# Kernel tuning notes

Hardware: AMD Instinct MI355X
Metric: run time of the kernel (lower is better)

## Reference

```python
import jax, jax.numpy as jnp
import numpy as np

B, N, HID, E, H = 4, 256, 256, 64, 4
OUT = HID // 2          # 128
D = OUT // H            # 32
AGG = H * (2 * D + 1)   # 260 = concat(mean D, attn_sum 1, max D) per head


def setup_inputs() -> dict:
    key = jax.random.key(0)
    ks = jax.random.split(key, 7)
    s = 0.05
    return {
        "h_x": jax.random.normal(ks[0], (B, N, HID), jnp.float32),
        "h_e": jax.random.normal(ks[1], (B, N, N, E), jnp.float32),
        "h_m": jnp.ones((B, N), jnp.float32),
        "W_Q": jax.random.normal(ks[2], (OUT, HID), jnp.float32) * s,
        "W_K": jax.random.normal(ks[3], (OUT, E), jnp.float32) * s,
        "W_V": jax.random.normal(ks[4], (OUT, E), jnp.float32) * s,
        "W_R": jax.random.normal(ks[5], (OUT, AGG), jnp.float32) * s,
    }


def reference(h_x, h_e, h_m, W_Q, W_K, W_V, W_R):
    # queries from node features: [B,H,N,D]
    h_q = (h_x @ W_Q.T).reshape(B, N, H, D).transpose(0, 2, 1, 3)
    # keys/values from dense pairwise edge features: [B,H,N,N,D]
    h_k = jnp.einsum('bnme,ce->bnmc', h_e, W_K).reshape(B, N, N, H, D).transpose(0, 3, 1, 2, 4)
    h_v = jnp.einsum('bnme,ce->bnmc', h_e, W_V).reshape(B, N, N, H, D).transpose(0, 3, 1, 2, 4)
    # broadcast dot: [B,H,N,N]
    scores = jnp.einsum('bhnd,bhnmd->bhnm', h_q, h_k) / np.float32(np.sqrt(D))
    # per-node mask broadcast as [B,1,N,1] (masks query rows)
    scores = jnp.where(h_m[:, None, :, None] == 0, -jnp.inf, scores)
    # NOTE: original code softmaxes over dim=1 = HEAD axis (faithful)
    attn = jax.nn.softmax(scores, axis=1)                      # [B,H,N,N]
    attn_w = attn[..., None] * h_v                             # [B,H,N,N,D]
    aggr_sum = attn_w.sum(axis=3)                              # [B,H,N,D]
    attn_sum = attn.sum(axis=3, keepdims=True) + 1e-8          # [B,H,N,1]
    aggr_mean = aggr_sum / attn_sum
    aggr_max = attn_w.max(axis=3)                              # [B,H,N,D]
    multi = jnp.concatenate([aggr_mean, attn_sum, aggr_max], axis=-1)  # [B,H,N,2D+1]
    aggr_out = multi.transpose(0, 2, 1, 3).reshape(B, N, AGG)  # [B,N,260]
    return aggr_out @ W_R.T                                    # [B,N,OUT]
```

## Files before the change

### kernel.cpp

```cpp
#include <hip/hip_runtime.h>
#include <hip/hip_bf16.h>

constexpr int Bb   = 4;
constexpr int Nn   = 256;
constexpr int HID  = 256;
constexpr int Ee   = 64;
constexpr int Hh   = 4;
constexpr int OUTc = 128;
constexpr int Dd   = 32;
constexpr int AGG  = 260;
constexpr int REC  = 264;
constexpr int QA_LD = 264;

constexpr size_t WS_WRT   = 0;
constexpr size_t WS_FRAGV = WS_WRT + (size_t)AGG * OUTc;
constexpr size_t WS_FRAGQ = WS_FRAGV + 4096;
constexpr size_t WS_UFRAG = WS_FRAGQ + 16384;

typedef __attribute__((ext_vector_type(8))) short short8;
typedef __attribute__((ext_vector_type(4))) float floatx4;

__device__ __forceinline__ unsigned pk2(float a, float b) {
    union { __hip_bfloat162 h; unsigned u; } cv;
    cv.h = __float22bfloat162_rn(float2{a, b});
    return cv.u;
}

__device__ __forceinline__ short8 pack8(floatx4 f0, floatx4 f1) {
    union { short8 s; unsigned u[4]; } r;
    r.u[0] = pk2(f0[0], f0[1]);
    r.u[1] = pk2(f0[2], f0[3]);
    r.u[2] = pk2(f1[0], f1[1]);
    r.u[3] = pk2(f1[2], f1[3]);
    return r.s;
}

__device__ __forceinline__ void gload16(const float* g, float* l) {
    __builtin_amdgcn_global_load_lds(
        (const __attribute__((address_space(1))) void*)g,
        (__attribute__((address_space(3))) void*)l, 16, 0, 0);
}

__global__ __launch_bounds__(256)
void eama_prep(const float* __restrict__ W_Q, const float* __restrict__ W_V,
               const float* __restrict__ W_R, const float* __restrict__ h_x,
               const float* __restrict__ W_K,
               unsigned short* __restrict__ wfragV, float* __restrict__ W_RT,
               unsigned short* __restrict__ ufrag)
{
    __shared__ __align__(16) unsigned short sA[16 * QA_LD];
    __shared__ __align__(16) float sqL[16][132];
    __shared__ __align__(16) float sU2[16][256];

    const int tid = threadIdx.x;
    const int bid = blockIdx.x;

    if (bid < 4) {
        const int e    = bid * 256 + tid;
        const int lane = e & 63;
        const int ks   = (e >> 6) & 1;
        const int ct   = e >> 7;
        const int ncol = lane & 15, q8 = lane >> 4;
        const float* row = W_V + (ct * 16 + ncol) * Ee;
        const int k0 = ks * 32 + q8 * 8;
        floatx4 f0 = *(const floatx4*)(row + k0);
        floatx4 f1 = *(const floatx4*)(row + k0 + 4);
        *(short8*)(wfragV + (size_t)e * 8) = pack8(f0, f1);
        return;
    }
    if (bid < 134) {
        const int i = (bid - 4) * 256 + tid;
        if (i < AGG * OUTc) {
            const int c = i & 127, j = i >> 7;
            W_RT[j * OUTc + c] = W_R[c * AGG + j];
        }
        return;
    }

    const int b0   = (bid - 134) * 16;
    const int lane = tid & 63;
    const int wv   = tid >> 6;
    const int ncol = lane & 15, q8 = lane >> 4;

    short8 bq[2][8];
    #pragma unroll
    for (int ct = 0; ct < 2; ++ct)
        #pragma unroll
        for (int ks = 0; ks < 8; ++ks) {
            const float* row = W_Q + (size_t)(wv * 32 + ct * 16 + ncol) * HID + ks * 32 + q8 * 8;
            bq[ct][ks] = pack8(*(const floatx4*)row, *(const floatx4*)(row + 4));
        }
    #pragma unroll
    for (int i = 0; i < 2; ++i) {
        const int idx = tid + i * 256;
        const int r = idx >> 5, blk = idx & 31;
        const float* src = h_x + (size_t)(b0 + r) * HID + blk * 8;
        floatx4 f0 = *(const floatx4*)(src);
        floatx4 f1 = *(const floatx4*)(src + 4);
        *(short8*)&sA[r * QA_LD + blk * 8] = pack8(f0, f1);
    }
    __syncthreads();
    floatx4 acc[2] = {(floatx4){0,0,0,0}, (floatx4){0,0,0,0}};
    #pragma unroll
    for (int ks = 0; ks < 8; ++ks) {
        short8 a = *(const short8*)&sA[ncol * QA_LD + ks * 32 + q8 * 8];
        acc[0] = __builtin_amdgcn_mfma_f32_16x16x32_bf16(a, bq[0][ks], acc[0], 0, 0, 0);
        acc[1] = __builtin_amdgcn_mfma_f32_16x16x32_bf16(a, bq[1][ks], acc[1], 0, 0, 0);
    }
    #pragma unroll
    for (int ct = 0; ct < 2; ++ct)
        #pragma unroll
        for (int rr = 0; rr < 4; ++rr)
            sqL[q8 * 4 + rr][wv * 32 + ct * 16 + ncol] = acc[ct][rr];
    __syncthreads();

    {
        const int h = wv, e = lane;
        float a16[16];
        #pragma unroll
        for (int i = 0; i < 16; ++i) a16[i] = 0.f;
        #pragma unroll
        for (int d4 = 0; d4 < 8; ++d4) {
            float wk0 = W_K[(h * Dd + d4 * 4 + 0) * Ee + e];
            float wk1 = W_K[(h * Dd + d4 * 4 + 1) * Ee + e];
            float wk2 = W_K[(h * Dd + d4 * 4 + 2) * Ee + e];
            float wk3 = W_K[(h * Dd + d4 * 4 + 3) * Ee + e];
            #pragma unroll
            for (int b16 = 0; b16 < 16; ++b16) {
                floatx4 qv = *(const floatx4*)&sqL[b16][h * Dd + d4 * 4];
                a16[b16] += (qv[0] * wk0 + qv[1] * wk1) + (qv[2] * wk2 + qv[3] * wk3);
            }
        }
        #pragma unroll
        for (int b16 = 0; b16 < 16; ++b16)
            sU2[b16][h * 64 + e] = a16[b16] * (0.1767766952966369f * 1.4426950408889634f);
    }
    __syncthreads();

    #pragma unroll
    for (int k = 0; k < 8; ++k) {
        const int ei   = tid + k * 256;
        const int b16  = ei >> 7;
        const int rest = ei & 127;
        const int ks   = rest >> 6;
        const int l    = rest & 63;
        const int nc   = l & 15, qq = l >> 4;
        short8 v = {0, 0, 0, 0, 0, 0, 0, 0};
        if (nc < Hh) {
            floatx4 f0 = *(const floatx4*)&sU2[b16][nc * 64 + ks * 32 + qq * 8];
            floatx4 f1 = *(const floatx4*)&sU2[b16][nc * 64 + ks * 32 + qq * 8 + 4];
            v = pack8(f0, f1);
        }
        *(short8*)(ufrag + ((size_t)((b0 + b16) * 2 + ks) * 64 + l) * 8) = v;
    }
}

__global__ __launch_bounds__(256, 2)
void eama_full(const float* __restrict__ h_e, const float* __restrict__ h_m,
               const unsigned short* __restrict__ wfragV,
               const unsigned short* __restrict__ ufrag,
               const float* __restrict__ W_RT, float* __restrict__ out)
{
    __shared__ __align__(16) float sStage[4][2][4][64][4];
    __shared__ __align__(16) float sS[4][16][4];
    __shared__ float sVS[4][OUTc];
    __shared__ float sVM[4][OUTc];
    __shared__ float sAS[4][Hh];
    __shared__ float sAsum[Hh];

    float* sM = &sStage[0][0][0][0][0];
    float (*sAcc)[OUTc] = (float (*)[OUTc])(sM + 384);

    const int tid  = threadIdx.x;
    const int lane = tid & 63;
    const int w    = tid >> 6;
    const int ncol = lane & 15;
    const int q8   = lane >> 4;
    const int bn   = blockIdx.x;
    const float maskv = h_m[bn];

    short8 bfV[8][2];
    #pragma unroll
    for (int ct = 0; ct < 8; ++ct)
        #pragma unroll
        for (int ks = 0; ks < 2; ++ks)
            bfV[ct][ks] = *(const short8*)(wfragV + ((size_t)(ct * 2 + ks) * 64 + lane) * 8);
    short8 bu0 = *(const short8*)(ufrag + ((size_t)(bn * 2 + 0) * 64 + lane) * 8);
    short8 bu1 = *(const short8*)(ufrag + ((size_t)(bn * 2 + 1) * 64 + lane) * 8);
    asm volatile("" ::: "memory");

    const float* heb = h_e + (size_t)bn * Nn * Ee;

    const int rl_s = lane >> 4;
    const int t_s  = ((lane & 15) - 5 * rl_s) & 15;
    const int soff = rl_s * 64 + t_s * 4;

    const int rl_c = ncol & 3;
    const int jc   = ncol >> 2;
    const int o0 = (rl_c * 16 + (((q8 * 2)     + 5 * rl_c) & 15)) * 4;
    const int o1 = (rl_c * 16 + (((q8 * 2 + 1) + 5 * rl_c) & 15)) * 4;
    const int o2 = (rl_c * 16 + (((q8 * 2 + 8) + 5 * rl_c) & 15)) * 4;
    const int o3 = (rl_c * 16 + (((q8 * 2 + 9) + 5 * rl_c) & 15)) * 4;

    #define STAGE(it_, buf_) do { \
        const float* ar_ = heb + (size_t)(w * 64 + (it_) * 16) * Ee + soff; \
        gload16(ar_,       &sStage[w][buf_][0][0][0]); \
        gload16(ar_ + 256, &sStage[w][buf_][1][0][0]); \
        gload16(ar_ + 512, &sStage[w][buf_][2][0][0]); \
        gload16(ar_ + 768, &sStage[w][buf_][3][0][0]); \
    } while (0)

    STAGE(0, 0);
    STAGE(1, 1);

    float vs[8], vm[8], asumH = 0.f;
    #pragma unroll
    for (int ct = 0; ct < 8; ++ct) { vs[ct] = 0.f; vm[ct] = -3.402823466e38f; }

    #pragma unroll
    for (int it = 0; it < 4; ++it) {
        const int buf = it & 1;
        if (it < 3) asm volatile("s_waitcnt vmcnt(4)" ::: "memory");
        else        asm volatile("s_waitcnt vmcnt(0)" ::: "memory");

        const float* chunkp = &sStage[w][buf][jc][0][0];
        floatx4 c0 = *(const floatx4*)(chunkp + o0);
        floatx4 c1 = *(const floatx4*)(chunkp + o1);
        floatx4 c2 = *(const floatx4*)(chunkp + o2);
        floatx4 c3 = *(const floatx4*)(chunkp + o3);
        short8 af0 = pack8(c0, c1);
        short8 af1 = pack8(c2, c3);
        if (it < 2) {
            asm volatile("s_waitcnt lgkmcnt(0)" ::: "memory");
            STAGE(it + 2, buf);
        }

        floatx4 accV[8], accS = (floatx4){0, 0, 0, 0};
        #pragma unroll
        for (int ct = 0; ct < 8; ++ct) accV[ct] = (floatx4){0, 0, 0, 0};
        __builtin_amdgcn_s_setprio(1);
        #pragma unroll
        for (int ct = 0; ct < 8; ++ct) {
            accV[ct] = __builtin_amdgcn_mfma_f32_16x16x32_bf16(af0, bfV[ct][0], accV[ct], 0, 0, 0);
            accV[ct] = __builtin_amdgcn_mfma_f32_16x16x32_bf16(af1, bfV[ct][1], accV[ct], 0, 0, 0);
        }
        accS = __builtin_amdgcn_mfma_f32_16x16x32_bf16(af0, bu0, accS, 0, 0, 0);
        accS = __builtin_amdgcn_mfma_f32_16x16x32_bf16(af1, bu1, accS, 0, 0, 0);
        __builtin_amdgcn_s_setprio(0);

        if (ncol < Hh) {
            #pragma unroll
            for (int r = 0; r < 4; ++r)
                sS[w][q8 * 4 + r][ncol] = (maskv != 0.f) ? accS[r] : -1e30f;
        }
        __builtin_amdgcn_wave_barrier();

        #pragma unroll
        for (int r = 0; r < 4; ++r) {
            floatx4 sc = *(const floatx4*)&sS[w][q8 * 4 + r][0];
            float e0 = __builtin_amdgcn_exp2f(sc[0]), e1 = __builtin_amdgcn_exp2f(sc[1]);
            float e2 = __builtin_amdgcn_exp2f(sc[2]), e3 = __builtin_amdgcn_exp2f(sc[3]);
            float inv = __builtin_amdgcn_rcpf((e0 + e1) + (e2 + e3));
            float a0 = e0 * inv, a1 = e1 * inv, a2 = e2 * inv, a3 = e3 * inv;
            asumH += (ncol & 2) ? ((ncol & 1) ? a3 : a2) : ((ncol & 1) ? a1 : a0);
            float p;
            p = a0 * accV[0][r]; vs[0] += p; vm[0] = fmaxf(vm[0], p);
            p = a0 * accV[1][r]; vs[1] += p; vm[1] = fmaxf(vm[1], p);
            p = a1 * accV[2][r]; vs[2] += p; vm[2] = fmaxf(vm[2], p);
            p = a1 * accV[3][r]; vs[3] += p; vm[3] = fmaxf(vm[3], p);
            p = a2 * accV[4][r]; vs[4] += p; vm[4] = fmaxf(vm[4], p);
            p = a2 * accV[5][r]; vs[5] += p; vm[5] = fmaxf(vm[5], p);
            p = a3 * accV[6][r]; vs[6] += p; vm[6] = fmaxf(vm[6], p);
            p = a3 * accV[7][r]; vs[7] += p; vm[7] = fmaxf(vm[7], p);
        }
        __builtin_amdgcn_wave_barrier();
    }
    #undef STAGE

    #pragma unroll
    for (int ct = 0; ct < 8; ++ct) {
        vs[ct] += __shfl_xor(vs[ct], 16, 64);
        vs[ct] += __shfl_xor(vs[ct], 32, 64);
        vm[ct] = fmaxf(vm[ct], __shfl_xor(vm[ct], 16, 64));
        vm[ct] = fmaxf(vm[ct], __shfl_xor(vm[ct], 32, 64));
    }
    asumH += __shfl_xor(asumH, 16, 64);
    asumH += __shfl_xor(asumH, 32, 64);

    if (lane < 16) {
        #pragma unroll
        for (int ct = 0; ct < 8; ++ct) {
            sVS[w][ct * 16 + lane] = vs[ct];
            sVM[w][ct * 16 + lane] = vm[ct];
        }
    }
    if (lane < Hh) sAS[w][lane] = asumH;
    __syncthreads();
    if (tid < Hh) {
        sAsum[tid] = 1e-8f +
            (sAS[0][tid] + sAS[1][tid]) + (sAS[2][tid] + sAS[3][tid]);
    }
    __syncthreads();
    if (tid < OUTc) {
        float vsum = (sVS[0][tid] + sVS[1][tid]) + (sVS[2][tid] + sVS[3][tid]);
        float vmax = fmaxf(fmaxf(sVM[0][tid], sVM[1][tid]), fmaxf(sVM[2][tid], sVM[3][tid]));
        const int h = tid >> 5, d = tid & 31;
        sM[h * 65 + d]      = vsum / sAsum[h];
        sM[h * 65 + 33 + d] = vmax;
        if (tid < Hh) sM[tid * 65 + 32] = sAsum[tid];
    }
    __syncthreads();
    {
        const int c = tid & 127, part = tid >> 7;
        const int j0 = part * 130;
        float a0 = 0.f, a1 = 0.f, a2 = 0.f, a3 = 0.f;
        #pragma unroll 4
        for (int j = j0; j < j0 + 128; j += 4) {
            a0 = fmaf(sM[j],     W_RT[(j)     * OUTc + c], a0);
            a1 = fmaf(sM[j + 1], W_RT[(j + 1) * OUTc + c], a1);
            a2 = fmaf(sM[j + 2], W_RT[(j + 2) * OUTc + c], a2);
            a3 = fmaf(sM[j + 3], W_RT[(j + 3) * OUTc + c], a3);
        }
        a0 = fmaf(sM[j0 + 128], W_RT[(j0 + 128) * OUTc + c], a0);
        a1 = fmaf(sM[j0 + 129], W_RT[(j0 + 129) * OUTc + c], a1);
        sAcc[part][c] = (a0 + a1) + (a2 + a3);
    }
    __syncthreads();
    if (tid < OUTc)
        out[bn * OUTc + tid] = sAcc[0][tid] + sAcc[1][tid];
}

extern "C" void kernel_launch(void* const* d_in, const int* in_sizes, int n_in,
                              void* d_out, int out_size, void* d_ws, size_t ws_size,
                              hipStream_t stream) {
    const float* h_x = (const float*)d_in[0];
    const float* h_e = (const float*)d_in[1];
    const float* h_m = (const float*)d_in[2];
    const float* W_Q = (const float*)d_in[3];
    const float* W_K = (const float*)d_in[4];
    const float* W_V = (const float*)d_in[5];
    const float* W_R = (const float*)d_in[6];
    float* out = (float*)d_out;

    float* ws            = (float*)d_ws;
    float* W_RT          = ws + WS_WRT;
    unsigned short* wfV  = (unsigned short*)(ws + WS_FRAGV);
    unsigned short* ufr  = (unsigned short*)(ws + WS_UFRAG);

    eama_prep<<<dim3(198), dim3(256), 0, stream>>>(W_Q, W_V, W_R, h_x, W_K, wfV, W_RT, ufr);
    eama_full<<<dim3(Bb * Nn), dim3(256), 0, stream>>>(h_e, h_m, wfV, ufr, W_RT, out);
}
```

Measured before the change: 124.5 us.

## Split each block's edge rows across eight waves and drop the reload pipeline

The fused kernel now launches 512 threads per block, so each of eight waves handles 32 edge rows (two 16-row chunks) instead of four waves each handling 64 rows. Both chunks are loaded into LDS up front, which removes the in-loop restaging and its wait. The per-block reduction and the final W_R projection are spread over eight waves and four output partial sums, reusing the staging buffer as scratch. The aim is more memory-level parallelism and less serial latency per block. In exchange the block uses twice the LDS and twice the threads, which can lower the number of resident blocks and adds more cross-wave reduction work.

```diff
diff --git a/kernel.cpp b/kernel.cpp
--- a/kernel.cpp
+++ b/kernel.cpp
@@ -9,7 +9,6 @@
 constexpr int OUTc = 128;
 constexpr int Dd   = 32;
 constexpr int AGG  = 260;
-constexpr int REC  = 264;
 constexpr int QA_LD = 264;
 
 constexpr size_t WS_WRT   = 0;
@@ -155,21 +154,14 @@
     }
 }
 
-__global__ __launch_bounds__(256, 2)
+__global__ __launch_bounds__(512, 2)
 void eama_full(const float* __restrict__ h_e, const float* __restrict__ h_m,
                const unsigned short* __restrict__ wfragV,
                const unsigned short* __restrict__ ufrag,
                const float* __restrict__ W_RT, float* __restrict__ out)
 {
-    __shared__ __align__(16) float sStage[4][2][4][64][4];
-    __shared__ __align__(16) float sS[4][16][4];
-    __shared__ float sVS[4][OUTc];
-    __shared__ float sVM[4][OUTc];
-    __shared__ float sAS[4][Hh];
-    __shared__ float sAsum[Hh];
-
-    float* sM = &sStage[0][0][0][0][0];
-    float (*sAcc)[OUTc] = (float (*)[OUTc])(sM + 384);
+    __shared__ __align__(16) float sStage[8][2][4][64][4];
+    __shared__ __align__(16) float sS[8][16][4];
 
     const int tid  = threadIdx.x;
     const int lane = tid & 63;
@@ -202,38 +194,33 @@
     const int o2 = (rl_c * 16 + (((q8 * 2 + 8) + 5 * rl_c) & 15)) * 4;
     const int o3 = (rl_c * 16 + (((q8 * 2 + 9) + 5 * rl_c) & 15)) * 4;
 
-    #define STAGE(it_, buf_) do { \
-        const float* ar_ = heb + (size_t)(w * 64 + (it_) * 16) * Ee + soff; \
-        gload16(ar_,       &sStage[w][buf_][0][0][0]); \
-        gload16(ar_ + 256, &sStage[w][buf_][1][0][0]); \
-        gload16(ar_ + 512, &sStage[w][buf_][2][0][0]); \
-        gload16(ar_ + 768, &sStage[w][buf_][3][0][0]); \
+    #define STAGE(it_) do { \
+        const float* ar_ = heb + (size_t)((w * 2 + (it_)) * 16) * Ee + soff; \
+        gload16(ar_,       &sStage[w][it_][0][0][0]); \
+        gload16(ar_ + 256, &sStage[w][it_][1][0][0]); \
+        gload16(ar_ + 512, &sStage[w][it_][2][0][0]); \
+        gload16(ar_ + 768, &sStage[w][it_][3][0][0]); \
     } while (0)
 
-    STAGE(0, 0);
-    STAGE(1, 1);
+    STAGE(0);
+    STAGE(1);
 
     float vs[8], vm[8], asumH = 0.f;
     #pragma unroll
     for (int ct = 0; ct < 8; ++ct) { vs[ct] = 0.f; vm[ct] = -3.402823466e38f; }
 
     #pragma unroll
-    for (int it = 0; it < 4; ++it) {
-        const int buf = it & 1;
-        if (it < 3) asm volatile("s_waitcnt vmcnt(4)" ::: "memory");
-        else        asm volatile("s_waitcnt vmcnt(0)" ::: "memory");
-
-        const float* chunkp = &sStage[w][buf][jc][0][0];
+    for (int it = 0; it < 2; ++it) {
+        if (it == 0) asm volatile("s_waitcnt vmcnt(4)" ::: "memory");
+        else         asm volatile("s_waitcnt vmcnt(0)" ::: "memory");
+
+        const float* chunkp = &sStage[w][it][jc][0][0];
         floatx4 c0 = *(const floatx4*)(chunkp + o0);
         floatx4 c1 = *(const floatx4*)(chunkp + o1);
         floatx4 c2 = *(const floatx4*)(chunkp + o2);
         floatx4 c3 = *(const floatx4*)(chunkp + o3);
         short8 af0 = pack8(c0, c1);
         short8 af1 = pack8(c2, c3);
-        if (it < 2) {
-            asm volatile("s_waitcnt lgkmcnt(0)" ::: "memory");
-            STAGE(it + 2, buf);
-        }
 
         floatx4 accV[8], accS = (floatx4){0, 0, 0, 0};
         #pragma unroll
@@ -287,47 +274,56 @@
     asumH += __shfl_xor(asumH, 16, 64);
     asumH += __shfl_xor(asumH, 32, 64);
 
+    float* SB = &sStage[0][0][0][0][0];
     if (lane < 16) {
         #pragma unroll
         for (int ct = 0; ct < 8; ++ct) {
-            sVS[w][ct * 16 + lane] = vs[ct];
-            sVM[w][ct * 16 + lane] = vm[ct];
-        }
-    }
-    if (lane < Hh) sAS[w][lane] = asumH;
+            SB[w * 2048 + ct * 16 + lane]       = vs[ct];
+            SB[w * 2048 + 128 + ct * 16 + lane] = vm[ct];
+        }
+    }
+    if (lane < Hh) SB[w * 2048 + 256 + lane] = asumH;
     __syncthreads();
     if (tid < Hh) {
-        sAsum[tid] = 1e-8f +
-            (sAS[0][tid] + sAS[1][tid]) + (sAS[2][tid] + sAS[3][tid]);
+        float s = 1e-8f;
+        #pragma unroll
+        for (int ww = 0; ww < 8; ++ww) s += SB[ww * 2048 + 256 + tid];
+        SB[512 + tid] = s;
     }
     __syncthreads();
     if (tid < OUTc) {
-        float vsum = (sVS[0][tid] + sVS[1][tid]) + (sVS[2][tid] + sVS[3][tid]);
-        float vmax = fmaxf(fmaxf(sVM[0][tid], sVM[1][tid]), fmaxf(sVM[2][tid], sVM[3][tid]));
+        float vsum = 0.f, vmax = -3.402823466e38f;
+        #pragma unroll
+        for (int ww = 0; ww < 8; ++ww) {
+            vsum += SB[ww * 2048 + tid];
+            vmax  = fmaxf(vmax, SB[ww * 2048 + 128 + tid]);
+        }
         const int h = tid >> 5, d = tid & 31;
-        sM[h * 65 + d]      = vsum / sAsum[h];
-        sM[h * 65 + 33 + d] = vmax;
-        if (tid < Hh) sM[tid * 65 + 32] = sAsum[tid];
+        SB[768 + h * 65 + d]      = vsum / SB[512 + h];
+        SB[768 + h * 65 + 33 + d] = vmax;
+        if (tid < Hh) SB[768 + tid * 65 + 32] = SB[512 + tid];
     }
     __syncthreads();
     {
         const int c = tid & 127, part = tid >> 7;
-        const int j0 = part * 130;
+        const int j0 = part * 65;
+        const float* sM = SB + 768;
         float a0 = 0.f, a1 = 0.f, a2 = 0.f, a3 = 0.f;
         #pragma unroll 4
-        for (int j = j0; j < j0 + 128; j += 4) {
+        for (int j = j0; j < j0 + 64; j += 4) {
             a0 = fmaf(sM[j],     W_RT[(j)     * OUTc + c], a0);
             a1 = fmaf(sM[j + 1], W_RT[(j + 1) * OUTc + c], a1);
             a2 = fmaf(sM[j + 2], W_RT[(j + 2) * OUTc + c], a2);
             a3 = fmaf(sM[j + 3], W_RT[(j + 3) * OUTc + c], a3);
         }
-        a0 = fmaf(sM[j0 + 128], W_RT[(j0 + 128) * OUTc + c], a0);
-        a1 = fmaf(sM[j0 + 129], W_RT[(j0 + 129) * OUTc + c], a1);
-        sAcc[part][c] = (a0 + a1) + (a2 + a3);
+        a0 = fmaf(sM[j0 + 64], W_RT[(j0 + 64) * OUTc + c], a0);
+        SB[1100 + part * 128 + c] = (a0 + a1) + (a2 + a3);
     }
     __syncthreads();
     if (tid < OUTc)
-        out[bn * OUTc + tid] = sAcc[0][tid] + sAcc[1][tid];
+        out[(size_t)bn * OUTc + tid] =
+            (SB[1100 + tid] + SB[1100 + 128 + tid]) +
+            (SB[1100 + 256 + tid] + SB[1100 + 384 + tid]);
 }
 
 extern "C" void kernel_launch(void* const* d_in, const int* in_sizes, int n_in,
@@ -348,5 +344,5 @@
     unsigned short* ufr  = (unsigned short*)(ws + WS_UFRAG);
 
     eama_prep<<<dim3(198), dim3(256), 0, stream>>>(W_Q, W_V, W_R, h_x, W_K, wfV, W_RT, ufr);
-    eama_full<<<dim3(Bb * Nn), dim3(256), 0, stream>>>(h_e, h_m, wfV, ufr, W_RT, out);
-}
+    eama_full<<<dim3(Bb * Nn), dim3(512), 0, stream>>>(h_e, h_m, wfV, ufr, W_RT, out);
+}
```

New measurement: 131.2 us. +5.3%, slower.

## Split each node's edge pass across two blocks and combine partials in a third kernel

Applied to the files above, without the earlier changes.

The main kernel now runs two blocks per (batch, node), each processing half of the 256 neighbours with both stages loaded up front, so there is no in-loop restaging. Partial sums, maxima and attention sums go to a workspace buffer. A new combine kernel merges them and applies W_R directly with vectorised row reads, which removes the W_R transpose from the prep kernel. This doubles the grid to raise occupancy and cut per-block latency, at the cost of an extra launch and a round-trip of partials through global memory.

```diff
diff --git a/kernel.cpp b/kernel.cpp
--- a/kernel.cpp
+++ b/kernel.cpp
@@ -12,13 +12,13 @@
 constexpr int REC  = 264;
 constexpr int QA_LD = 264;
 
-constexpr size_t WS_WRT   = 0;
-constexpr size_t WS_FRAGV = WS_WRT + (size_t)AGG * OUTc;
-constexpr size_t WS_FRAGQ = WS_FRAGV + 4096;
-constexpr size_t WS_UFRAG = WS_FRAGQ + 16384;
+constexpr size_t WS_FRAGV = 33280;
+constexpr size_t WS_UFRAG = 53760;
+constexpr size_t WS_PART  = 600000;
 
 typedef __attribute__((ext_vector_type(8))) short short8;
 typedef __attribute__((ext_vector_type(4))) float floatx4;
+typedef __attribute__((ext_vector_type(2))) float floatx2;
 
 __device__ __forceinline__ unsigned pk2(float a, float b) {
     union { __hip_bfloat162 h; unsigned u; } cv;
@@ -43,10 +43,8 @@
 
 __global__ __launch_bounds__(256)
 void eama_prep(const float* __restrict__ W_Q, const float* __restrict__ W_V,
-               const float* __restrict__ W_R, const float* __restrict__ h_x,
-               const float* __restrict__ W_K,
-               unsigned short* __restrict__ wfragV, float* __restrict__ W_RT,
-               unsigned short* __restrict__ ufrag)
+               const float* __restrict__ h_x, const float* __restrict__ W_K,
+               unsigned short* __restrict__ wfragV, unsigned short* __restrict__ ufrag)
 {
     __shared__ __align__(16) unsigned short sA[16 * QA_LD];
     __shared__ __align__(16) float sqL[16][132];
@@ -68,16 +66,8 @@
         *(short8*)(wfragV + (size_t)e * 8) = pack8(f0, f1);
         return;
     }
-    if (bid < 134) {
-        const int i = (bid - 4) * 256 + tid;
-        if (i < AGG * OUTc) {
-            const int c = i & 127, j = i >> 7;
-            W_RT[j * OUTc + c] = W_R[c * AGG + j];
-        }
-        return;
-    }
-
-    const int b0   = (bid - 134) * 16;
+
+    const int b0   = (bid - 4) * 16;
     const int lane = tid & 63;
     const int wv   = tid >> 6;
     const int ncol = lane & 15, q8 = lane >> 4;
@@ -156,27 +146,24 @@
 }
 
 __global__ __launch_bounds__(256, 2)
-void eama_full(const float* __restrict__ h_e, const float* __restrict__ h_m,
+void eama_half(const float* __restrict__ h_e, const float* __restrict__ h_m,
                const unsigned short* __restrict__ wfragV,
                const unsigned short* __restrict__ ufrag,
-               const float* __restrict__ W_RT, float* __restrict__ out)
+               float* __restrict__ part)
 {
     __shared__ __align__(16) float sStage[4][2][4][64][4];
     __shared__ __align__(16) float sS[4][16][4];
     __shared__ float sVS[4][OUTc];
     __shared__ float sVM[4][OUTc];
     __shared__ float sAS[4][Hh];
-    __shared__ float sAsum[Hh];
-
-    float* sM = &sStage[0][0][0][0][0];
-    float (*sAcc)[OUTc] = (float (*)[OUTc])(sM + 384);
 
     const int tid  = threadIdx.x;
     const int lane = tid & 63;
     const int w    = tid >> 6;
     const int ncol = lane & 15;
     const int q8   = lane >> 4;
-    const int bn   = blockIdx.x;
+    const int bn   = blockIdx.x >> 1;
+    const int half = blockIdx.x & 1;
     const float maskv = h_m[bn];
 
     short8 bfV[8][2];
@@ -202,38 +189,33 @@
     const int o2 = (rl_c * 16 + (((q8 * 2 + 8) + 5 * rl_c) & 15)) * 4;
     const int o3 = (rl_c * 16 + (((q8 * 2 + 9) + 5 * rl_c) & 15)) * 4;
 
-    #define STAGE(it_, buf_) do { \
-        const float* ar_ = heb + (size_t)(w * 64 + (it_) * 16) * Ee + soff; \
-        gload16(ar_,       &sStage[w][buf_][0][0][0]); \
-        gload16(ar_ + 256, &sStage[w][buf_][1][0][0]); \
-        gload16(ar_ + 512, &sStage[w][buf_][2][0][0]); \
-        gload16(ar_ + 768, &sStage[w][buf_][3][0][0]); \
+    #define STAGE(it_) do { \
+        const float* ar_ = heb + (size_t)(half * 128 + w * 32 + (it_) * 16) * Ee + soff; \
+        gload16(ar_,       &sStage[w][it_][0][0][0]); \
+        gload16(ar_ + 256, &sStage[w][it_][1][0][0]); \
+        gload16(ar_ + 512, &sStage[w][it_][2][0][0]); \
+        gload16(ar_ + 768, &sStage[w][it_][3][0][0]); \
     } while (0)
 
-    STAGE(0, 0);
-    STAGE(1, 1);
+    STAGE(0);
+    STAGE(1);
 
     float vs[8], vm[8], asumH = 0.f;
     #pragma unroll
     for (int ct = 0; ct < 8; ++ct) { vs[ct] = 0.f; vm[ct] = -3.402823466e38f; }
 
     #pragma unroll
-    for (int it = 0; it < 4; ++it) {
-        const int buf = it & 1;
-        if (it < 3) asm volatile("s_waitcnt vmcnt(4)" ::: "memory");
-        else        asm volatile("s_waitcnt vmcnt(0)" ::: "memory");
-
-        const float* chunkp = &sStage[w][buf][jc][0][0];
+    for (int it = 0; it < 2; ++it) {
+        if (it == 0) asm volatile("s_waitcnt vmcnt(4)" ::: "memory");
+        else         asm volatile("s_waitcnt vmcnt(0)" ::: "memory");
+
+        const float* chunkp = &sStage[w][it][jc][0][0];
         floatx4 c0 = *(const floatx4*)(chunkp + o0);
         floatx4 c1 = *(const floatx4*)(chunkp + o1);
         floatx4 c2 = *(const floatx4*)(chunkp + o2);
         floatx4 c3 = *(const floatx4*)(chunkp + o3);
         short8 af0 = pack8(c0, c1);
         short8 af1 = pack8(c2, c3);
-        if (it < 2) {
-            asm volatile("s_waitcnt lgkmcnt(0)" ::: "memory");
-            STAGE(it + 2, buf);
-        }
 
         floatx4 accV[8], accS = (floatx4){0, 0, 0, 0};
         #pragma unroll
@@ -296,14 +278,35 @@
     }
     if (lane < Hh) sAS[w][lane] = asumH;
     __syncthreads();
-    if (tid < Hh) {
-        sAsum[tid] = 1e-8f +
-            (sAS[0][tid] + sAS[1][tid]) + (sAS[2][tid] + sAS[3][tid]);
-    }
-    __syncthreads();
+
+    float* P = part + (size_t)(bn * 2 + half) * REC;
     if (tid < OUTc) {
-        float vsum = (sVS[0][tid] + sVS[1][tid]) + (sVS[2][tid] + sVS[3][tid]);
-        float vmax = fmaxf(fmaxf(sVM[0][tid], sVM[1][tid]), fmaxf(sVM[2][tid], sVM[3][tid]));
+        P[tid]       = (sVS[0][tid] + sVS[1][tid]) + (sVS[2][tid] + sVS[3][tid]);
+        P[128 + tid] = fmaxf(fmaxf(sVM[0][tid], sVM[1][tid]),
+                             fmaxf(sVM[2][tid], sVM[3][tid]));
+        if (tid < Hh)
+            P[256 + tid] = (sAS[0][tid] + sAS[1][tid]) + (sAS[2][tid] + sAS[3][tid]);
+    }
+}
+
+__global__ __launch_bounds__(256)
+void eama_comb(const float* __restrict__ part, const float* __restrict__ W_R,
+               float* __restrict__ out)
+{
+    __shared__ __align__(16) float sM[REC];
+    __shared__ float sAsum[Hh];
+    __shared__ float sAcc[2][OUTc];
+
+    const int tid = threadIdx.x;
+    const int bn  = blockIdx.x;
+    const float* A = part + (size_t)(bn * 2 + 0) * REC;
+    const float* B = part + (size_t)(bn * 2 + 1) * REC;
+
+    if (tid < Hh) sAsum[tid] = 1e-8f + A[256 + tid] + B[256 + tid];
+    __syncthreads();
+    if (tid < OUTc) {
+        float vsum = A[tid] + B[tid];
+        float vmax = fmaxf(A[128 + tid], B[128 + tid]);
         const int h = tid >> 5, d = tid & 31;
         sM[h * 65 + d]      = vsum / sAsum[h];
         sM[h * 65 + 33 + d] = vmax;
@@ -311,23 +314,27 @@
     }
     __syncthreads();
     {
-        const int c = tid & 127, part = tid >> 7;
-        const int j0 = part * 130;
+        const int c = tid & 127, p = tid >> 7;
+        const int j0 = p * 130;
+        const float* wr = W_R + (size_t)c * AGG + j0;
         float a0 = 0.f, a1 = 0.f, a2 = 0.f, a3 = 0.f;
-        #pragma unroll 4
-        for (int j = j0; j < j0 + 128; j += 4) {
-            a0 = fmaf(sM[j],     W_RT[(j)     * OUTc + c], a0);
-            a1 = fmaf(sM[j + 1], W_RT[(j + 1) * OUTc + c], a1);
-            a2 = fmaf(sM[j + 2], W_RT[(j + 2) * OUTc + c], a2);
-            a3 = fmaf(sM[j + 3], W_RT[(j + 3) * OUTc + c], a3);
-        }
-        a0 = fmaf(sM[j0 + 128], W_RT[(j0 + 128) * OUTc + c], a0);
-        a1 = fmaf(sM[j0 + 129], W_RT[(j0 + 129) * OUTc + c], a1);
-        sAcc[part][c] = (a0 + a1) + (a2 + a3);
+        #pragma unroll 8
+        for (int j = 0; j < 128; j += 4) {
+            floatx2 X = *(const floatx2*)(wr + j);
+            floatx2 Y = *(const floatx2*)(wr + j + 2);
+            a0 = fmaf(sM[j0 + j],     X[0], a0);
+            a1 = fmaf(sM[j0 + j + 1], X[1], a1);
+            a2 = fmaf(sM[j0 + j + 2], Y[0], a2);
+            a3 = fmaf(sM[j0 + j + 3], Y[1], a3);
+        }
+        floatx2 T = *(const floatx2*)(wr + 128);
+        a0 = fmaf(sM[j0 + 128], T[0], a0);
+        a1 = fmaf(sM[j0 + 129], T[1], a1);
+        sAcc[p][c] = (a0 + a1) + (a2 + a3);
     }
     __syncthreads();
     if (tid < OUTc)
-        out[bn * OUTc + tid] = sAcc[0][tid] + sAcc[1][tid];
+        out[(size_t)bn * OUTc + tid] = sAcc[0][tid] + sAcc[1][tid];
 }
 
 extern "C" void kernel_launch(void* const* d_in, const int* in_sizes, int n_in,
@@ -343,10 +350,11 @@
     float* out = (float*)d_out;
 
     float* ws            = (float*)d_ws;
-    float* W_RT          = ws + WS_WRT;
     unsigned short* wfV  = (unsigned short*)(ws + WS_FRAGV);
     unsigned short* ufr  = (unsigned short*)(ws + WS_UFRAG);
-
-    eama_prep<<<dim3(198), dim3(256), 0, stream>>>(W_Q, W_V, W_R, h_x, W_K, wfV, W_RT, ufr);
-    eama_full<<<dim3(Bb * Nn), dim3(256), 0, stream>>>(h_e, h_m, wfV, ufr, W_RT, out);
-}
+    float* part          = ws + WS_PART;
+
+    eama_prep<<<dim3(68),      dim3(256), 0, stream>>>(W_Q, W_V, h_x, W_K, wfV, ufr);
+    eama_half<<<dim3(2 * Bb * Nn), dim3(256), 0, stream>>>(h_e, h_m, wfV, ufr, part);
+    eama_comb<<<dim3(Bb * Nn), dim3(256), 0, stream>>>(part, W_R, out);
+}
```

After: 133.4 us. +7.1%, slower.
